# Kernel tuning notes

Measured on AMD Instinct MI355X. Metric: run time of the kernel, lower is better.

Reference implementation:

```python
import jax, jax.numpy as jnp
import numpy as np

D, C, H, W = 8, 512, 64, 64


def setup_inputs() -> dict:
    key = jax.random.key(0)
    k1, k2, k3 = jax.random.split(key, 3)
    x = jax.random.normal(k1, (D, C, H, W), dtype=jnp.float32)
    atten = jax.random.normal(k2, (D, C, C), dtype=jnp.float32)
    gamma = jax.random.normal(k3, (1,), dtype=jnp.float32)
    return {"x": x, "atten": atten, "gamma": gamma}


def reference(x, atten, gamma):
    d, c, h, w = x.shape
    q = x.reshape(d, c, h * w)              # q == v == flattened x; k = q^T
    # energy[d, i, j] = <channel_i, channel_j> over spatial positions
    energy = jnp.einsum('din,djn->dij', q, q)
    # max-centering: rowmax - energy (note the sign flip vs standard softmax)
    energy_new = jnp.max(energy, axis=-1, keepdims=True) - energy
    attention = jax.nn.softmax(energy_new, axis=-1)
    attention = jax.nn.softmax(attention + atten, axis=-1)
    # out = attention^T @ v : out[d, j, n] = sum_i attention[d, i, j] * v[d, i, n]
    out = jnp.einsum('dij,din->djn', attention, q).reshape(d, c, h, w)
    return gamma * out + x
```

## Files before the change

### kernel.cpp

```cpp
#include <hip/hip_runtime.h>
#include <hip/hip_bf16.h>

#define DD 8
#define CC 512
#define NN 4096

typedef __bf16 bf16x8 __attribute__((ext_vector_type(8)));
typedef float  f32x4  __attribute__((ext_vector_type(4)));
typedef ushort ush8   __attribute__((ext_vector_type(8)));

__device__ __forceinline__ ushort f2bf(float f) {
  unsigned u = __float_as_uint(f);
  u = (u + 0x7fffu + ((u >> 16) & 1u)) >> 16;
  return (ushort)u;
}
__device__ __forceinline__ float bf2f(ushort h) {
  return __uint_as_float(((unsigned)h) << 16);
}

__device__ __forceinline__ void gl_lds16(const ushort* g, ushort* l) {
  __builtin_amdgcn_global_load_lds(
      (const __attribute__((address_space(1))) void*)g,
      (__attribute__((address_space(3))) void*)l, 16, 0, 0);
}


__global__ __launch_bounds__(256) void k0_convert(
    const float* __restrict__ x, ushort* __restrict__ qh,
    ushort* __restrict__ ql, ushort* __restrict__ qt) {
  int d = blockIdx.z, ct = blockIdx.y, nt = blockIdx.x;
  __shared__ ushort T[64][68];
  int t = threadIdx.x;
  int rr = t >> 4;
  int c4 = (t & 15) * 4;
  const float* xb = x + ((size_t)(d * CC + ct * 64)) * NN + nt * 64;
#pragma unroll
  for (int it = 0; it < 4; ++it) {
    int r = it * 16 + rr;
    float4 v = *(const float4*)(xb + (size_t)r * NN + c4);
    ushort h0 = f2bf(v.x), h1 = f2bf(v.y), h2 = f2bf(v.z), h3 = f2bf(v.w);
    ushort l0 = f2bf(v.x - bf2f(h0)), l1 = f2bf(v.y - bf2f(h1));
    ushort l2 = f2bf(v.z - bf2f(h2)), l3 = f2bf(v.w - bf2f(h3));
    size_t qi = ((size_t)(d * CC + ct * 64 + r)) * NN + nt * 64 + c4;
    *(ushort4*)(qh + qi) = make_ushort4(h0, h1, h2, h3);
    *(ushort4*)(ql + qi) = make_ushort4(l0, l1, l2, l3);
    *(ushort4*)&T[r][c4] = make_ushort4(h0, h1, h2, h3);
  }
  __syncthreads();
#pragma unroll
  for (int it = 0; it < 4; ++it) {
    int nl = it * 16 + rr;
    ushort4 v = make_ushort4(T[c4 + 0][nl], T[c4 + 1][nl], T[c4 + 2][nl], T[c4 + 3][nl]);
    *(ushort4*)(qt + ((size_t)(d * NN + nt * 64 + nl)) * CC + ct * 64 + c4) = v;
  }
}

__global__ __launch_bounds__(256, 2) void k1_gram(
    const ushort* __restrict__ qh, const ushort* __restrict__ ql,
    float* __restrict__ Ep, int ns, int nkk, int ksp) {
  __shared__ ushort As[2][128 * 32];
  __shared__ ushort Bs[2][128 * 32];
  int b = blockIdx.x;
  int s = b % ns;
  int rem = b / ns;
  int tile = rem % 10, d = rem / 10;
  int tm = (int)((0x3221110000ULL >> (tile * 4)) & 15ULL);
  int tn = (int)((0x3323213210ULL >> (tile * 4)) & 15ULL);
  int t = threadIdx.x, lane = t & 63, w = t >> 6;
  int wm = (w >> 1) * 64, wn = (w & 1) * 64;
  int qd = lane >> 4, fr = lane & 15;
  int qo = (qd ^ ((fr >> 1) & 3)) * 8;
  int so = ((lane & 3) ^ ((lane >> 3) & 3)) * 8;

  const ushort* srcbase = (w & 1) ? ql : qh;
  int rowblk = (w < 2) ? tm : tn;
  const ushort* gsrc = srcbase +
      ((size_t)(d * CC + rowblk * 128 + (lane >> 2))) * NN +
      (size_t)s * ksp + so;
  ushort* ldst = (w < 2) ? As[w & 1] : Bs[w & 1];

  f32x4 acc[4][4];
#pragma unroll
  for (int i = 0; i < 4; ++i)
#pragma unroll
    for (int j = 0; j < 4; ++j) acc[i][j] = (f32x4){0.f, 0.f, 0.f, 0.f};

  for (int kk = 0; kk < nkk; ++kk) {
    __syncthreads();
    const ushort* g0 = gsrc + (size_t)kk * 32;
#pragma unroll
    for (int c = 0; c < 8; ++c)
      gl_lds16(g0 + (size_t)c * 16 * NN, ldst + c * 512);
    __syncthreads();

    bf16x8 ah[4], al[4];
#pragma unroll
    for (int mi = 0; mi < 4; ++mi) {
      int off = (wm + mi * 16 + fr) * 32 + qo;
      ah[mi] = *(const bf16x8*)&As[0][off];
      al[mi] = *(const bf16x8*)&As[1][off];
    }
#pragma unroll
    for (int ni = 0; ni < 4; ++ni) {
      int off = (wn + ni * 16 + fr) * 32 + qo;
      bf16x8 bh = *(const bf16x8*)&Bs[0][off];
      bf16x8 bl = *(const bf16x8*)&Bs[1][off];
#pragma unroll
      for (int mi = 0; mi < 4; ++mi) {
        acc[mi][ni] = __builtin_amdgcn_mfma_f32_16x16x32_bf16(ah[mi], bh, acc[mi][ni], 0, 0, 0);
        acc[mi][ni] = __builtin_amdgcn_mfma_f32_16x16x32_bf16(ah[mi], bl, acc[mi][ni], 0, 0, 0);
        acc[mi][ni] = __builtin_amdgcn_mfma_f32_16x16x32_bf16(al[mi], bh, acc[mi][ni], 0, 0, 0);
      }
    }
  }

  size_t ebase = ((size_t)(s * DD + d)) * ((size_t)CC * CC);
#pragma unroll
  for (int mi = 0; mi < 4; ++mi) {
    int r0 = tm * 128 + wm + mi * 16 + qd * 4;
#pragma unroll
    for (int ni = 0; ni < 4; ++ni) {
      int c0 = tn * 128 + wn + ni * 16 + fr;
      float* ep = Ep + ebase + (size_t)r0 * CC + c0;
#pragma unroll
      for (int r = 0; r < 4; ++r) ep[(size_t)r * CC] = acc[mi][ni][r];
    }
  }
  if (tm != tn) {
#pragma unroll
    for (int mi = 0; mi < 4; ++mi) {
      int r0 = tm * 128 + wm + mi * 16 + qd * 4;
#pragma unroll
      for (int ni = 0; ni < 4; ++ni) {
        int c0 = tn * 128 + wn + ni * 16 + fr;
        float4 v = make_float4(acc[mi][ni][0], acc[mi][ni][1],
                               acc[mi][ni][2], acc[mi][ni][3]);
        *(float4*)(Ep + ebase + (size_t)c0 * CC + r0) = v;
      }
    }
  }
}

__device__ __forceinline__ float wmin(float v) {
#pragma unroll
  for (int o = 32; o > 0; o >>= 1) v = fminf(v, __shfl_xor(v, o));
  return v;
}
__device__ __forceinline__ float wmax(float v) {
#pragma unroll
  for (int o = 32; o > 0; o >>= 1) v = fmaxf(v, __shfl_xor(v, o));
  return v;
}
__device__ __forceinline__ float wsum(float v) {
#pragma unroll
  for (int o = 32; o > 0; o >>= 1) v += __shfl_xor(v, o);
  return v;
}

__global__ __launch_bounds__(256) void k2_softmax(
    const float* __restrict__ Ep, const float* __restrict__ atten,
    ushort* __restrict__ a2t, int ns) {
  int d = blockIdx.y, i0 = blockIdx.x * 8;
  int t = threadIdx.x, lane = t & 63, w = t >> 6;
  int j8 = lane * 8;
  __shared__ ushort T[8][520];
  const size_t SP = (size_t)DD * CC * CC;

#pragma unroll
  for (int r2 = 0; r2 < 2; ++r2) {
    int ri = w * 2 + r2;
    size_t base = ((size_t)(d * CC + i0 + ri)) * CC + j8;
    f32x4 a0 = (f32x4){0.f, 0.f, 0.f, 0.f};
    f32x4 a1 = (f32x4){0.f, 0.f, 0.f, 0.f};
    for (int s = 0; s < ns; ++s) {
      const float* p = Ep + (size_t)s * SP + base;
      a0 += *(const f32x4*)p;
      a1 += *(const f32x4*)(p + 4);
    }
    float mn = fminf(fminf(fminf(a0[0], a0[1]), fminf(a0[2], a0[3])),
                     fminf(fminf(a1[0], a1[1]), fminf(a1[2], a1[3])));
    mn = wmin(mn);
    float p0 = __expf(mn - a0[0]), p1 = __expf(mn - a0[1]);
    float p2 = __expf(mn - a0[2]), p3 = __expf(mn - a0[3]);
    float p4 = __expf(mn - a1[0]), p5 = __expf(mn - a1[1]);
    float p6 = __expf(mn - a1[2]), p7 = __expf(mn - a1[3]);
    float s1 = wsum(p0 + p1 + p2 + p3 + p4 + p5 + p6 + p7);
    float inv1 = 1.0f / s1;
    const float* ap = atten + base;
    f32x4 t0 = *(const f32x4*)ap;
    f32x4 t1 = *(const f32x4*)(ap + 4);
    float u0 = p0 * inv1 + t0[0], u1 = p1 * inv1 + t0[1];
    float u2 = p2 * inv1 + t0[2], u3 = p3 * inv1 + t0[3];
    float u4 = p4 * inv1 + t1[0], u5 = p5 * inv1 + t1[1];
    float u6 = p6 * inv1 + t1[2], u7 = p7 * inv1 + t1[3];
    float mx = wmax(fmaxf(fmaxf(fmaxf(u0, u1), fmaxf(u2, u3)),
                          fmaxf(fmaxf(u4, u5), fmaxf(u6, u7))));
    float q0 = __expf(u0 - mx), q1 = __expf(u1 - mx);
    float q2 = __expf(u2 - mx), q3 = __expf(u3 - mx);
    float q4 = __expf(u4 - mx), q5 = __expf(u5 - mx);
    float q6 = __expf(u6 - mx), q7 = __expf(u7 - mx);
    float s2 = wsum(q0 + q1 + q2 + q3 + q4 + q5 + q6 + q7);
    float inv2 = 1.0f / s2;
    ush8 o;
    o[0] = f2bf(q0 * inv2); o[1] = f2bf(q1 * inv2);
    o[2] = f2bf(q2 * inv2); o[3] = f2bf(q3 * inv2);
    o[4] = f2bf(q4 * inv2); o[5] = f2bf(q5 * inv2);
    o[6] = f2bf(q6 * inv2); o[7] = f2bf(q7 * inv2);
    *(ush8*)&T[ri][j8] = o;
  }
  __syncthreads();
#pragma unroll
  for (int it = 0; it < 2; ++it) {
    int j = t + it * 256;
    ush8 o;
#pragma unroll
    for (int k = 0; k < 8; ++k) o[k] = T[k][j];
    *(ush8*)&a2t[((size_t)(d * CC + j)) * CC + i0] = o;
  }
}

#define K3_COMPUTE(SOFF)                                                       \
  {                                                                            \
    bf16x8 qf[4];                                                              \
    _Pragma("unroll")                                                          \
    for (int ii = 0; ii < 4; ++ii)                                             \
      qf[ii] = *(const bf16x8*)&Bs[(SOFF) + (wn2 + ii * 16 + fr) * 32 + qo];   \
    _Pragma("unroll")                                                          \
    for (int jj = 0; jj < 4; ++jj) {                                           \
      bf16x8 af = *(const bf16x8*)&As[(SOFF) + (wj + jj * 16 + fr) * 32 + qo]; \
      _Pragma("unroll")                                                        \
      for (int ii = 0; ii < 4; ++ii)                                           \
        acc[ii][jj] = __builtin_amdgcn_mfma_f32_16x16x32_bf16(                 \
            qf[ii], af, acc[ii][jj], 0, 0, 0);                                 \
    }                                                                          \
  }

#define K3_STAGE(S)                                                            \
  {                                                                            \
    ushort* ls = mylds + ((S) & 3) * 4096;                                     \
    const ushort* gs = g0 + (size_t)(S) * 32;                                  \
    _Pragma("unroll")                                                          \
    for (int c = 0; c < 4; ++c)                                                \
      gl_lds16(gs + (size_t)(c * 16) * CC, ls + c * 512);                      \
  }

__global__ __launch_bounds__(256, 2) void k3_out(
    const ushort* __restrict__ a2t, const ushort* __restrict__ qt,
    const float* __restrict__ x, const float* __restrict__ gamma,
    float* __restrict__ out) {
  __shared__ ushort As[4 * 128 * 32];
  __shared__ ushort Bs[4 * 128 * 32];
  int b = blockIdx.x;
  int nt = b & 31, jt = (b >> 5) & 3, d = b >> 7;
  int t = threadIdx.x, lane = t & 63, w = t >> 6;
  int wj = (w >> 1) * 64, wn2 = (w & 1) * 64;
  int qd = lane >> 4, fr = lane & 15;
  int qo = (qd ^ ((fr >> 1) & 3)) * 8;
  int so = ((lane & 3) ^ ((lane >> 3) & 3)) * 8;

  const ushort* src = (w < 2)
      ? (a2t + (size_t)d * CC * CC + (size_t)(jt * 128) * CC)
      : (qt + (size_t)d * NN * CC + (size_t)(nt * 128) * CC);
  int cbase = (w & 1) * 4;
  const ushort* g0 = src + ((size_t)(cbase * 16 + (lane >> 2))) * CC + so;
  ushort* mylds = ((w < 2) ? As : Bs) + cbase * 512;

  f32x4 acc[4][4];
#pragma unroll
  for (int i = 0; i < 4; ++i)
#pragma unroll
    for (int j = 0; j < 4; ++j) acc[i][j] = (f32x4){0.f, 0.f, 0.f, 0.f};

  K3_STAGE(0)
  K3_STAGE(1)
  K3_STAGE(2)

#pragma unroll 1
  for (int kk = 0; kk < 13; ++kk) {
    asm volatile("s_waitcnt vmcnt(8)\n\ts_barrier" ::: "memory");
    K3_STAGE(kk + 3)
    K3_COMPUTE((kk & 3) * 4096)
  }
  asm volatile("s_waitcnt vmcnt(8)\n\ts_barrier" ::: "memory");
  K3_COMPUTE(1 * 4096)
  asm volatile("s_waitcnt vmcnt(4)\n\ts_barrier" ::: "memory");
  K3_COMPUTE(2 * 4096)
  asm volatile("s_waitcnt vmcnt(0)\n\ts_barrier" ::: "memory");

  int n0b = nt * 128 + wn2 + qd * 4;
  float4 xp0[4], xp1[4];
#pragma unroll
  for (int jj = 0; jj < 4; ++jj) {
    size_t rb = ((size_t)(d * CC + jt * 128 + wj + jj * 16 + fr)) * NN;
    xp0[jj] = *(const float4*)(x + rb + n0b);
    xp1[jj] = *(const float4*)(x + rb + n0b + 16);
  }
  K3_COMPUTE(3 * 4096)

  float g = gamma[0];
  float4 x2[4], x3[4];
#pragma unroll
  for (int jj = 0; jj < 4; ++jj)
    x2[jj] = *(const float4*)(x + ((size_t)(d * CC + jt * 128 + wj + jj * 16 + fr)) * NN + n0b + 32);
#pragma unroll
  for (int jj = 0; jj < 4; ++jj) {
    size_t idx = ((size_t)(d * CC + jt * 128 + wj + jj * 16 + fr)) * NN + n0b;
    *(float4*)(out + idx) = make_float4(g * acc[0][jj][0] + xp0[jj].x,
                                        g * acc[0][jj][1] + xp0[jj].y,
                                        g * acc[0][jj][2] + xp0[jj].z,
                                        g * acc[0][jj][3] + xp0[jj].w);
  }
#pragma unroll
  for (int jj = 0; jj < 4; ++jj)
    x3[jj] = *(const float4*)(x + ((size_t)(d * CC + jt * 128 + wj + jj * 16 + fr)) * NN + n0b + 48);
#pragma unroll
  for (int jj = 0; jj < 4; ++jj) {
    size_t idx = ((size_t)(d * CC + jt * 128 + wj + jj * 16 + fr)) * NN + n0b + 16;
    *(float4*)(out + idx) = make_float4(g * acc[1][jj][0] + xp1[jj].x,
                                        g * acc[1][jj][1] + xp1[jj].y,
                                        g * acc[1][jj][2] + xp1[jj].z,
                                        g * acc[1][jj][3] + xp1[jj].w);
  }
#pragma unroll
  for (int jj = 0; jj < 4; ++jj) {
    size_t idx = ((size_t)(d * CC + jt * 128 + wj + jj * 16 + fr)) * NN + n0b + 32;
    *(float4*)(out + idx) = make_float4(g * acc[2][jj][0] + x2[jj].x,
                                        g * acc[2][jj][1] + x2[jj].y,
                                        g * acc[2][jj][2] + x2[jj].z,
                                        g * acc[2][jj][3] + x2[jj].w);
  }
#pragma unroll
  for (int jj = 0; jj < 4; ++jj) {
    size_t idx = ((size_t)(d * CC + jt * 128 + wj + jj * 16 + fr)) * NN + n0b + 48;
    *(float4*)(out + idx) = make_float4(g * acc[3][jj][0] + x3[jj].x,
                                        g * acc[3][jj][1] + x3[jj].y,
                                        g * acc[3][jj][2] + x3[jj].z,
                                        g * acc[3][jj][3] + x3[jj].w);
  }
}

extern "C" void kernel_launch(void* const* d_in, const int* in_sizes, int n_in,
                              void* d_out, int out_size, void* d_ws, size_t ws_size,
                              hipStream_t stream) {
  (void)in_sizes; (void)n_in; (void)out_size;
  const float* x     = (const float*)d_in[0];
  const float* atten = (const float*)d_in[1];
  const float* gamma = (const float*)d_in[2];
  float* out = (float*)d_out;

  char* ws = (char*)d_ws;
  ushort* qh  = (ushort*)(ws);
  ushort* ql  = (ushort*)(ws + 33554432);
  ushort* qt  = (ushort*)(ws + 67108864);
  ushort* a2t = (ushort*)(ws + 100663296);
  float*  Ep  = (float*) (ws + 104857600);

  int ns = (ws_size >= 104857600ULL + 8ULL * 8388608ULL) ? 8 : 4;
  int ksp = NN / ns;
  int nkk = ksp / 32;

  k0_convert<<<dim3(64, 8, 8), 256, 0, stream>>>(x, qh, ql, qt);
  k1_gram   <<<dim3(80 * ns), 256, 0, stream>>>(qh, ql, Ep, ns, nkk, ksp);
  k2_softmax<<<dim3(64, 8), 256, 0, stream>>>(Ep, atten, a2t, ns);
  k3_out    <<<dim3(1024), 256, 0, stream>>>(a2t, qt, x, gamma, out);
}
```

Baseline: 232.8 us.

## Double-buffer gram kernel LDS loads and split output kernel launch

The gram kernel now uses a two-stage LDS ring, issuing the async global-to-LDS loads for the next K slice before computing on the current one. Raw s_waitcnt/s_barrier asm replaces __syncthreads so the loads overlap the MFMA work. LDS per block doubles, which may limit occupancy, and the hand-written vmcnt counts must match the issued loads. Separately, the output kernel is split into two launches over halves of the batch, which adds launch overhead with no obvious overlap benefit.

```diff
diff --git a/kernel.cpp b/kernel.cpp
--- a/kernel.cpp
+++ b/kernel.cpp
@@ -55,11 +55,43 @@
   }
 }
 
+#define K1_STAGE(S)                                                            \
+  {                                                                            \
+    ushort* ls = lbase + ((S) & 1) * 8192;                                     \
+    const ushort* gs = gsrc + (size_t)(S) * 32;                                \
+    _Pragma("unroll")                                                          \
+    for (int c = 0; c < 8; ++c)                                                \
+      gl_lds16(gs + (size_t)c * 16 * NN, ls + c * 512);                        \
+  }
+
+#define K1_COMPUTE(SOFF)                                                       \
+  {                                                                            \
+    bf16x8 ah[4], al[4];                                                       \
+    _Pragma("unroll")                                                          \
+    for (int mi = 0; mi < 4; ++mi) {                                           \
+      int off = (SOFF) + (wm + mi * 16 + fr) * 32 + qo;                        \
+      ah[mi] = *(const bf16x8*)&As[off];                                       \
+      al[mi] = *(const bf16x8*)&As[off + 4096];                                \
+    }                                                                          \
+    _Pragma("unroll")                                                          \
+    for (int ni = 0; ni < 4; ++ni) {                                           \
+      int off = (SOFF) + (wn + ni * 16 + fr) * 32 + qo;                        \
+      bf16x8 bh = *(const bf16x8*)&Bs[off];                                    \
+      bf16x8 bl = *(const bf16x8*)&Bs[off + 4096];                             \
+      _Pragma("unroll")                                                        \
+      for (int mi = 0; mi < 4; ++mi) {                                         \
+        acc[mi][ni] = __builtin_amdgcn_mfma_f32_16x16x32_bf16(ah[mi], bh, acc[mi][ni], 0, 0, 0); \
+        acc[mi][ni] = __builtin_amdgcn_mfma_f32_16x16x32_bf16(ah[mi], bl, acc[mi][ni], 0, 0, 0); \
+        acc[mi][ni] = __builtin_amdgcn_mfma_f32_16x16x32_bf16(al[mi], bh, acc[mi][ni], 0, 0, 0); \
+      }                                                                        \
+    }                                                                          \
+  }
+
 __global__ __launch_bounds__(256, 2) void k1_gram(
     const ushort* __restrict__ qh, const ushort* __restrict__ ql,
     float* __restrict__ Ep, int ns, int nkk, int ksp) {
-  __shared__ ushort As[2][128 * 32];
-  __shared__ ushort Bs[2][128 * 32];
+  __shared__ ushort As[2 * 2 * 4096];
+  __shared__ ushort Bs[2 * 2 * 4096];
   int b = blockIdx.x;
   int s = b % ns;
   int rem = b / ns;
@@ -77,7 +109,7 @@
   const ushort* gsrc = srcbase +
       ((size_t)(d * CC + rowblk * 128 + (lane >> 2))) * NN +
       (size_t)s * ksp + so;
-  ushort* ldst = (w < 2) ? As[w & 1] : Bs[w & 1];
+  ushort* lbase = ((w < 2) ? As : Bs) + (w & 1) * 4096;
 
   f32x4 acc[4][4];
 #pragma unroll
@@ -85,34 +117,17 @@
 #pragma unroll
     for (int j = 0; j < 4; ++j) acc[i][j] = (f32x4){0.f, 0.f, 0.f, 0.f};
 
-  for (int kk = 0; kk < nkk; ++kk) {
-    __syncthreads();
-    const ushort* g0 = gsrc + (size_t)kk * 32;
-#pragma unroll
-    for (int c = 0; c < 8; ++c)
-      gl_lds16(g0 + (size_t)c * 16 * NN, ldst + c * 512);
-    __syncthreads();
-
-    bf16x8 ah[4], al[4];
-#pragma unroll
-    for (int mi = 0; mi < 4; ++mi) {
-      int off = (wm + mi * 16 + fr) * 32 + qo;
-      ah[mi] = *(const bf16x8*)&As[0][off];
-      al[mi] = *(const bf16x8*)&As[1][off];
-    }
-#pragma unroll
-    for (int ni = 0; ni < 4; ++ni) {
-      int off = (wn + ni * 16 + fr) * 32 + qo;
-      bf16x8 bh = *(const bf16x8*)&Bs[0][off];
-      bf16x8 bl = *(const bf16x8*)&Bs[1][off];
-#pragma unroll
-      for (int mi = 0; mi < 4; ++mi) {
-        acc[mi][ni] = __builtin_amdgcn_mfma_f32_16x16x32_bf16(ah[mi], bh, acc[mi][ni], 0, 0, 0);
-        acc[mi][ni] = __builtin_amdgcn_mfma_f32_16x16x32_bf16(ah[mi], bl, acc[mi][ni], 0, 0, 0);
-        acc[mi][ni] = __builtin_amdgcn_mfma_f32_16x16x32_bf16(al[mi], bh, acc[mi][ni], 0, 0, 0);
-      }
-    }
-  }
+  K1_STAGE(0)
+
+#pragma unroll 1
+  for (int kk = 0; kk < nkk - 1; ++kk) {
+    asm volatile("s_waitcnt lgkmcnt(0)\n\ts_barrier" ::: "memory");
+    K1_STAGE(kk + 1)
+    asm volatile("s_waitcnt vmcnt(8)\n\ts_barrier" ::: "memory");
+    K1_COMPUTE((kk & 1) * 8192)
+  }
+  asm volatile("s_waitcnt vmcnt(0) lgkmcnt(0)\n\ts_barrier" ::: "memory");
+  K1_COMPUTE(((nkk - 1) & 1) * 8192)
 
   size_t ebase = ((size_t)(s * DD + d)) * ((size_t)CC * CC);
 #pragma unroll
@@ -247,11 +262,11 @@
 __global__ __launch_bounds__(256, 2) void k3_out(
     const ushort* __restrict__ a2t, const ushort* __restrict__ qt,
     const float* __restrict__ x, const float* __restrict__ gamma,
-    float* __restrict__ out) {
+    float* __restrict__ out, int d0) {
   __shared__ ushort As[4 * 128 * 32];
   __shared__ ushort Bs[4 * 128 * 32];
   int b = blockIdx.x;
-  int nt = b & 31, jt = (b >> 5) & 3, d = b >> 7;
+  int nt = b & 31, jt = (b >> 5) & 3, d = d0 + (b >> 7);
   int t = threadIdx.x, lane = t & 63, w = t >> 6;
   int wj = (w >> 1) * 64, wn2 = (w & 1) * 64;
   int qd = lane >> 4, fr = lane & 15;
@@ -362,5 +377,6 @@
   k0_convert<<<dim3(64, 8, 8), 256, 0, stream>>>(x, qh, ql, qt);
   k1_gram   <<<dim3(80 * ns), 256, 0, stream>>>(qh, ql, Ep, ns, nkk, ksp);
   k2_softmax<<<dim3(64, 8), 256, 0, stream>>>(Ep, atten, a2t, ns);
-  k3_out    <<<dim3(1024), 256, 0, stream>>>(a2t, qt, x, gamma, out);
-}
+  k3_out    <<<dim3(512), 256, 0, stream>>>(a2t, qt, x, gamma, out, 0);
+  k3_out    <<<dim3(512), 256, 0, stream>>>(a2t, qt, x, gamma, out, 4);
+}
```

New measurement: 239.9 us. 3.0% more time.
